# Performance work log

Measured on AMD Instinct MI355X. Metric: run time of the kernel, lower is better.

The kernel has to match this reference:

```python
import jax, jax.numpy as jnp
import numpy as np

H, KD, VD = 8, 64, 64
W = 1.25  # custom weight scale


def layer_norm(x, g, b, eps=1e-5):
    m = x.mean(-1, keepdims=True)
    v = ((x - m) ** 2).mean(-1, keepdims=True)
    return (x - m) * jax.lax.rsqrt(v + eps) * g + b


def cross_attention(x1, x2, wq, wk, wv, wo, bo, wm):
    # Conv1d kernel_size=1 == matmul; channel axis splits as (heads, dim)
    b, s1, _ = x1.shape
    s2 = x2.shape[1]
    q = (x1 @ wq.T).reshape(b, s1, H, KD).transpose(0, 2, 1, 3)  # bhqk
    k = (x2 @ wk.T).reshape(b, s2, H, KD).transpose(0, 2, 1, 3)
    v = (x2 @ wv.T).reshape(b, s2, H, VD).transpose(0, 2, 1, 3)
    attn = jnp.einsum('bhqd,bhsd->bhqs', q, k) * (1.0 / (KD ** 0.5))
    attn = jax.nn.softmax(attn * wm, axis=-1)  # elementwise weight BEFORE softmax
    o = jnp.einsum('bhqs,bhsv->bhqv', attn, v)
    o = o.transpose(0, 2, 1, 3).reshape(b, s1, H * VD)
    return o @ wo.T + bo


def make_wm1(nvars, sl2, patch_num):
    sl = sl2 // 2
    wm = jnp.ones((nvars, sl2), jnp.float32)
    wm = wm.at[:2 * patch_num, :sl].multiply(W)
    wm = wm.at[2 * patch_num:, sl:].multiply(W)
    return wm[None, None]  # broadcast over batch, heads


def make_wm2(nvars, sv, patch_num, patch_num_v):
    wm = jnp.ones((nvars, sv), jnp.float32)
    wm = wm.at[:patch_num, :patch_num_v].multiply(W)
    wm = wm.at[patch_num:2 * patch_num, patch_num_v:2 * patch_num_v].multiply(W)
    wm = wm.at[2 * patch_num:, 2 * patch_num_v:].multiply(W)
    return wm[None, None]


def forward(cords_features, spatial_features, speed_features,
            wq1, wk1, wv1, wo1, bo1, wq2, wk2, wv2, wo2, bo2,
            ln1_g, ln1_b, ln2_g, ln2_b, ln3_g, ln3_b,
            ffn_w1, ffn_b1, ffn_w2, ffn_b2):
    b, nvars, d = cords_features.shape
    patch_num = nvars // 3
    patch_num_v = speed_features.shape[1] // 3
    wm1 = make_wm1(nvars, spatial_features.shape[1], patch_num)
    wm2 = make_wm2(nvars, 3 * patch_num_v, patch_num, patch_num_v)
    x = cross_attention(cords_features, spatial_features, wq1, wk1, wv1, wo1, bo1, wm1)
    x = layer_norm(x + cords_features, ln1_g, ln1_b)
    r2 = x
    x = cross_attention(x, speed_features, wq2, wk2, wv2, wo2, bo2, wm2)
    x = layer_norm(x + r2, ln2_g, ln2_b)
    r3 = x
    h = jax.nn.gelu(x @ ffn_w1.T + ffn_b1, approximate=False)
    x = h @ ffn_w2.T + ffn_b2
    return layer_norm(x + r3, ln3_g, ln3_b)


def setup_inputs():
    key = jax.random.key(0)
    ks = jax.random.split(key, 16)
    D, DF = 512, 2048
    s = 0.02
    inp = {
        'cords_features': jax.random.normal(ks[0], (8, 768, D), jnp.float32),
        'spatial_features': jax.random.normal(ks[1], (8, 1024, D), jnp.float32),
        'speed_features': jax.random.normal(ks[2], (8, 768, D), jnp.float32),
        'wq1': jax.random.normal(ks[3], (H * KD, D)) * s,
        'wk1': jax.random.normal(ks[4], (H * KD, D)) * s,
        'wv1': jax.random.normal(ks[5], (H * VD, D)) * s,
        'wo1': jax.random.normal(ks[6], (D, H * VD)) * s,
        'bo1': jnp.zeros((D,), jnp.float32),
        'wq2': jax.random.normal(ks[7], (H * KD, D)) * s,
        'wk2': jax.random.normal(ks[8], (H * KD, D)) * s,
        'wv2': jax.random.normal(ks[9], (H * VD, D)) * s,
        'wo2': jax.random.normal(ks[10], (D, H * VD)) * s,
        'bo2': jnp.zeros((D,), jnp.float32),
        'ln1_g': jnp.ones((D,), jnp.float32), 'ln1_b': jnp.zeros((D,), jnp.float32),
        'ln2_g': jnp.ones((D,), jnp.float32), 'ln2_b': jnp.zeros((D,), jnp.float32),
        'ln3_g': jnp.ones((D,), jnp.float32), 'ln3_b': jnp.zeros((D,), jnp.float32),
        'ffn_w1': jax.random.normal(ks[11], (DF, D)) * s,
        'ffn_b1': jnp.zeros((DF,), jnp.float32),
        'ffn_w2': jax.random.normal(ks[12], (D, DF)) * s,
        'ffn_b2': jnp.zeros((D,), jnp.float32),
    }
    return inp


def reference(cords_features, spatial_features, speed_features,
              wq1, wk1, wv1, wo1, bo1, wq2, wk2, wv2, wo2, bo2,
              ln1_g, ln1_b, ln2_g, ln2_b, ln3_g, ln3_b,
              ffn_w1, ffn_b1, ffn_w2, ffn_b2):
    return forward(cords_features, spatial_features, speed_features,
                   wq1, wk1, wv1, wo1, bo1, wq2, wk2, wv2, wo2, bo2,
                   ln1_g, ln1_b, ln2_g, ln2_b, ln3_g, ln3_b,
                   ffn_w1, ffn_b1, ffn_w2, ffn_b2)
```

## Files before the change

### kernel.cpp

```cpp
#include <hip/hip_runtime.h>
#include <hip/hip_bf16.h>


#define LN_EPS 1e-5f
#define WSCALE 1.25f

typedef __attribute__((ext_vector_type(8))) short short8;
typedef __attribute__((ext_vector_type(4))) float floatx4;
typedef unsigned short us;

__device__ __forceinline__ float bf2f(us u) {
    union { unsigned int i; float f; } v; v.i = ((unsigned int)u) << 16; return v.f;
}
__device__ __forceinline__ us f2bf(float f) {
    union { float f; unsigned int i; } v; v.f = f;
    return (us)((v.i + 0x7FFFu + ((v.i >> 16) & 1u)) >> 16);
}
__device__ __forceinline__ float gelu_f(float v) {
    float x  = v * 0.70710678118654752f;
    float ax = fabsf(x);
    float t  = 1.0f / (1.0f + 0.3275911f * ax);
    float p  = t * (0.254829592f + t * (-0.284496736f + t * (1.421413741f +
               t * (-1.453152027f + t * 1.061405429f))));
    float er = 1.0f - p * __expf(-ax * ax);
    er = copysignf(er, x);
    return 0.5f * v * (1.0f + er);
}

__device__ __forceinline__ int xcd_swizzle_lid()
{
    int nwg = gridDim.x * gridDim.y;
    int lid = blockIdx.y * gridDim.x + blockIdx.x;
    int cpx = nwg >> 3;
    return (lid & 7) * cpx + (lid >> 3);
}

struct CastArgs {
    const float* src[13];
    us* dst[13];
    int blk_ofs[14];
};
__global__ __launch_bounds__(256) void cast_all(CastArgs a)
{
    int b = blockIdx.x;
    int e = 0;
    while (b >= a.blk_ofs[e + 1]) ++e;
    int i = ((b - a.blk_ofs[e]) * 256 + threadIdx.x) * 8;
    const float* s = a.src[e];
    us* d = a.dst[e];
    float4 x = *(const float4*)(s + i);
    float4 y = *(const float4*)(s + i + 4);
    *(ushort4*)(d + i)     = make_ushort4(f2bf(x.x), f2bf(x.y), f2bf(x.z), f2bf(x.w));
    *(ushort4*)(d + i + 4) = make_ushort4(f2bf(y.x), f2bf(y.y), f2bf(y.z), f2bf(y.w));
}

__global__ __launch_bounds__(256) void gemm_r64(
    const us* __restrict__ A, const us* __restrict__ Bw,
    const float* __restrict__ bias, us* __restrict__ Cb,
    int M, int N, int K, int flags)
{
    constexpr int BM = 128, BN = 64;
    constexpr int SLOT = (BM + BN) * 64;
    __shared__ us L[3 * SLOT];

    int t = threadIdx.x;
    int wave = t >> 6, lane = t & 63;

    int swz = xcd_swizzle_lid();
    int gx = gridDim.x;
    int m0 = (swz / gx) * BM, n0 = (swz % gx) * BN;

    int wr = wave * 32;

    int r_in = lane >> 3, pq = lane & 7;
    const us* gA[4]; int lA[4];
#pragma unroll
    for (int c = 0; c < 4; ++c) {
        int r = 32 * c + 8 * wave + r_in;
        int q = pq ^ (r & 7);
        gA[c] = A + (size_t)(m0 + r) * K + 8 * q;
        lA[c] = (32 * c + 8 * wave) * 64;
    }
    const us* gB[2]; int lB[2];
#pragma unroll
    for (int c = 0; c < 2; ++c) {
        int r = 32 * c + 8 * wave + r_in;
        int q = pq ^ (r & 7);
        gB[c] = Bw + (size_t)(n0 + r) * K + 8 * q;
        lB[c] = BM * 64 + (32 * c + 8 * wave) * 64;
    }

    int fcol = lane & 15, fj = lane >> 4;
    int aoff[2][2], boff[4][2];
#pragma unroll
    for (int mt = 0; mt < 2; ++mt)
#pragma unroll
        for (int kc = 0; kc < 2; ++kc) {
            int fr = wr + 16 * mt + fcol;
            aoff[mt][kc] = fr * 64 + ((kc * 4 + fj) ^ (fr & 7)) * 8;
        }
#pragma unroll
    for (int nt = 0; nt < 4; ++nt)
#pragma unroll
        for (int kc = 0; kc < 2; ++kc) {
            int br = 16 * nt + fcol;
            boff[nt][kc] = BM * 64 + br * 64 + ((kc * 4 + fj) ^ (br & 7)) * 8;
        }

    floatx4 acc[2][4] = {};

    auto stage_p0 = [&](int slot, int kt) {
        us* base = L + slot * SLOT;
#pragma unroll
        for (int c = 0; c < 3; ++c)
            __builtin_amdgcn_global_load_lds(
                (const __attribute__((address_space(1))) void*)(gA[c] + (size_t)kt * 64),
                (__attribute__((address_space(3))) void*)(base + lA[c]), 16, 0, 0);
    };
    auto stage_p1 = [&](int slot, int kt) {
        us* base = L + slot * SLOT;
        __builtin_amdgcn_global_load_lds(
            (const __attribute__((address_space(1))) void*)(gA[3] + (size_t)kt * 64),
            (__attribute__((address_space(3))) void*)(base + lA[3]), 16, 0, 0);
#pragma unroll
        for (int c = 0; c < 2; ++c)
            __builtin_amdgcn_global_load_lds(
                (const __attribute__((address_space(1))) void*)(gB[c] + (size_t)kt * 64),
                (__attribute__((address_space(3))) void*)(base + lB[c]), 16, 0, 0);
    };

    int ktrips = K >> 6;
    stage_p0(0, 0); stage_p1(0, 0);
    if (ktrips > 1) {
        stage_p0(1, 1); stage_p1(1, 1);
        asm volatile("s_waitcnt vmcnt(6)" ::: "memory");
    } else {
        asm volatile("s_waitcnt vmcnt(0)" ::: "memory");
    }
    __builtin_amdgcn_s_barrier();
    asm volatile("" ::: "memory");

    int cs = 0;
    for (int tt = 0; tt < ktrips; ++tt) {
        int ns = cs + 2; if (ns >= 3) ns -= 3;
        bool pre = (tt + 2) < ktrips;
        const us* base = L + cs * SLOT;

        if (pre) stage_p0(ns, tt + 2);
        {
            short8 af[2], bfv[4];
#pragma unroll
            for (int mt = 0; mt < 2; ++mt) af[mt] = *(const short8*)(base + aoff[mt][0]);
#pragma unroll
            for (int nt = 0; nt < 4; ++nt) bfv[nt] = *(const short8*)(base + boff[nt][0]);
            __builtin_amdgcn_s_setprio(1);
#pragma unroll
            for (int mt = 0; mt < 2; ++mt)
#pragma unroll
                for (int nt = 0; nt < 4; ++nt)
                    acc[mt][nt] = __builtin_amdgcn_mfma_f32_16x16x32_bf16(
                        af[mt], bfv[nt], acc[mt][nt], 0, 0, 0);
            __builtin_amdgcn_s_setprio(0);
        }

        if (pre) stage_p1(ns, tt + 2);
        {
            short8 af[2], bfv[4];
#pragma unroll
            for (int mt = 0; mt < 2; ++mt) af[mt] = *(const short8*)(base + aoff[mt][1]);
#pragma unroll
            for (int nt = 0; nt < 4; ++nt) bfv[nt] = *(const short8*)(base + boff[nt][1]);
            __builtin_amdgcn_s_setprio(1);
#pragma unroll
            for (int mt = 0; mt < 2; ++mt)
#pragma unroll
                for (int nt = 0; nt < 4; ++nt)
                    acc[mt][nt] = __builtin_amdgcn_mfma_f32_16x16x32_bf16(
                        af[mt], bfv[nt], acc[mt][nt], 0, 0, 0);
            __builtin_amdgcn_s_setprio(0);
        }

        if (tt + 1 < ktrips) {
            if (pre) asm volatile("s_waitcnt vmcnt(6)" ::: "memory");
            else     asm volatile("s_waitcnt vmcnt(0)" ::: "memory");
            __builtin_amdgcn_s_barrier();
            asm volatile("" ::: "memory");
        }
        cs = cs + 1; if (cs >= 3) cs = 0;
    }

    int rq = lane >> 4;
#pragma unroll
    for (int mt = 0; mt < 2; ++mt)
#pragma unroll
        for (int nt = 0; nt < 4; ++nt) {
            int col = n0 + 16 * nt + fcol;
            float bv = (flags & 1) ? bias[col] : 0.f;
#pragma unroll
            for (int r = 0; r < 4; ++r) {
                int row = m0 + wr + 16 * mt + rq * 4 + r;
                float v = acc[mt][nt][r] + bv;
                if (flags & 2) v = gelu_f(v);
                Cb[(size_t)row * N + col] = f2bf(v);
            }
        }
}

template<int BM, int BN>
__global__ __launch_bounds__(512, 2) void gemm_ring(
    const us* __restrict__ A, const us* __restrict__ Bw,
    const float* __restrict__ bias, us* __restrict__ Cb,
    int M, int N, int K, int flags, int vS, us* __restrict__ Vtg)
{
    static_assert(BM == 256 && BN == 128, "gemm_ring fixed at 256x128");
    constexpr int SLOT = (BM + BN) * 64;
    __shared__ us L[3 * SLOT];

    int t = threadIdx.x;
    int wave = t >> 6, lane = t & 63;

    int swz = xcd_swizzle_lid();
    int gx = gridDim.x;
    int m0 = (swz / gx) * BM, n0 = (swz % gx) * BN;

    int wr = (wave >> 1) * 64, wc = (wave & 1) * 64;

    int r_in = lane >> 3, pq = lane & 7;
    const us* gA[4]; int lA[4];
#pragma unroll
    for (int c = 0; c < 4; ++c) {
        int r = 64 * c + 8 * wave + r_in;
        int q = pq ^ (r & 7);
        gA[c] = A + (size_t)(m0 + r) * K + 8 * q;
        lA[c] = (64 * c + 8 * wave) * 64;
    }
    const us* gB[2]; int lB[2];
#pragma unroll
    for (int c = 0; c < 2; ++c) {
        int r = 64 * c + 8 * wave + r_in;
        int q = pq ^ (r & 7);
        gB[c] = Bw + (size_t)(n0 + r) * K + 8 * q;
        lB[c] = BM * 64 + (64 * c + 8 * wave) * 64;
    }

    int fcol = lane & 15, fj = lane >> 4;
    int aoff[4][2], boff[4][2];
#pragma unroll
    for (int mt = 0; mt < 4; ++mt)
#pragma unroll
        for (int kc = 0; kc < 2; ++kc) {
            int fr = wr + 16 * mt + fcol;
            aoff[mt][kc] = fr * 64 + ((kc * 4 + fj) ^ (fr & 7)) * 8;
        }
#pragma unroll
    for (int nt = 0; nt < 4; ++nt)
#pragma unroll
        for (int kc = 0; kc < 2; ++kc) {
            int br = wc + 16 * nt + fcol;
            boff[nt][kc] = BM * 64 + br * 64 + ((kc * 4 + fj) ^ (br & 7)) * 8;
        }

    floatx4 acc[4][4] = {};

    auto stage_p0 = [&](int slot, int kt) {
        us* base = L + slot * SLOT;
#pragma unroll
        for (int c = 0; c < 3; ++c)
            __builtin_amdgcn_global_load_lds(
                (const __attribute__((address_space(1))) void*)(gA[c] + (size_t)kt * 64),
                (__attribute__((address_space(3))) void*)(base + lA[c]), 16, 0, 0);
    };
    auto stage_p1 = [&](int slot, int kt) {
        us* base = L + slot * SLOT;
        __builtin_amdgcn_global_load_lds(
            (const __attribute__((address_space(1))) void*)(gA[3] + (size_t)kt * 64),
            (__attribute__((address_space(3))) void*)(base + lA[3]), 16, 0, 0);
#pragma unroll
        for (int c = 0; c < 2; ++c)
            __builtin_amdgcn_global_load_lds(
                (const __attribute__((address_space(1))) void*)(gB[c] + (size_t)kt * 64),
                (__attribute__((address_space(3))) void*)(base + lB[c]), 16, 0, 0);
    };

    int ktrips = K >> 6;
    stage_p0(0, 0); stage_p1(0, 0);
    if (ktrips > 1) {
        stage_p0(1, 1); stage_p1(1, 1);
        asm volatile("s_waitcnt vmcnt(6)" ::: "memory");
    } else {
        asm volatile("s_waitcnt vmcnt(0)" ::: "memory");
    }
    __builtin_amdgcn_s_barrier();
    asm volatile("" ::: "memory");

    int cs = 0;
    for (int tt = 0; tt < ktrips; ++tt) {
        int ns = cs + 2; if (ns >= 3) ns -= 3;
        bool pre = (tt + 2) < ktrips;
        const us* base = L + cs * SLOT;

        if (pre) stage_p0(ns, tt + 2);
        {
            short8 af[4], bfv[4];
#pragma unroll
            for (int mt = 0; mt < 4; ++mt) af[mt] = *(const short8*)(base + aoff[mt][0]);
#pragma unroll
            for (int nt = 0; nt < 4; ++nt) bfv[nt] = *(const short8*)(base + boff[nt][0]);
            __builtin_amdgcn_s_setprio(1);
#pragma unroll
            for (int mt = 0; mt < 4; ++mt)
#pragma unroll
                for (int nt = 0; nt < 4; ++nt)
                    acc[mt][nt] = __builtin_amdgcn_mfma_f32_16x16x32_bf16(
                        af[mt], bfv[nt], acc[mt][nt], 0, 0, 0);
            __builtin_amdgcn_s_setprio(0);
        }

        if (pre) stage_p1(ns, tt + 2);
        {
            short8 af[4], bfv[4];
#pragma unroll
            for (int mt = 0; mt < 4; ++mt) af[mt] = *(const short8*)(base + aoff[mt][1]);
#pragma unroll
            for (int nt = 0; nt < 4; ++nt) bfv[nt] = *(const short8*)(base + boff[nt][1]);
            __builtin_amdgcn_s_setprio(1);
#pragma unroll
            for (int mt = 0; mt < 4; ++mt)
#pragma unroll
                for (int nt = 0; nt < 4; ++nt)
                    acc[mt][nt] = __builtin_amdgcn_mfma_f32_16x16x32_bf16(
                        af[mt], bfv[nt], acc[mt][nt], 0, 0, 0);
            __builtin_amdgcn_s_setprio(0);
        }

        if (tt + 1 < ktrips) {
            if (pre) asm volatile("s_waitcnt vmcnt(6)" ::: "memory");
            else     asm volatile("s_waitcnt vmcnt(0)" ::: "memory");
            __builtin_amdgcn_s_barrier();
            asm volatile("" ::: "memory");
        }
        cs = cs + 1; if (cs >= 3) cs = 0;
    }

    int rq = lane >> 4;
    if (flags & 8) {
        int b = m0 / vS;
        int s_base = m0 - b * vS;
        if (n0 < 512) {
#pragma unroll
            for (int mt = 0; mt < 4; ++mt)
#pragma unroll
                for (int nt = 0; nt < 4; ++nt) {
                    int col = n0 + wc + 16 * nt + fcol;
#pragma unroll
                    for (int r = 0; r < 4; ++r) {
                        int rloc = wr + 16 * mt + rq * 4 + r;
                        Cb[(size_t)(m0 + rloc) * 512 + col] = f2bf(acc[mt][nt][r]);
                    }
                }
        } else {
#pragma unroll
            for (int mt = 0; mt < 4; ++mt)
#pragma unroll
                for (int nt = 0; nt < 4; ++nt) {
                    int cv = n0 + wc + 16 * nt + fcol - 512;
                    int hv = cv >> 6, dv = cv & 63;
                    int sb = s_base + wr + 16 * mt + rq * 4;
                    ushort4 pk = make_ushort4(
                        f2bf(acc[mt][nt][0]), f2bf(acc[mt][nt][1]),
                        f2bf(acc[mt][nt][2]), f2bf(acc[mt][nt][3]));
                    *(ushort4*)(Vtg + ((size_t)(b * 8 + hv) * 64 + dv) * vS + sb) = pk;
                }
        }
        return;
    }

#pragma unroll
    for (int mt = 0; mt < 4; ++mt)
#pragma unroll
        for (int nt = 0; nt < 4; ++nt) {
            int col = n0 + wc + 16 * nt + fcol;
            float bv = (flags & 1) ? bias[col] : 0.f;
#pragma unroll
            for (int r = 0; r < 4; ++r) {
                int row = m0 + wr + 16 * mt + rq * 4 + r;
                float v = acc[mt][nt][r] + bv;
                if (flags & 2) v = gelu_f(v);
                Cb[(size_t)row * N + col] = f2bf(v);
            }
        }
}

__global__ __launch_bounds__(256, 3) void attn_kernel(
    const us* __restrict__ Q, const us* __restrict__ Kf,
    const us* __restrict__ Vg, us* __restrict__ O,
    int S1, int S2, int shift)
{
    __shared__ us Qs[64 * 64];
    __shared__ us Ks[2][64 * 64];
    __shared__ us Vs[2][64 * 64];
    __shared__ us Ps[64 * 72];

    int t = threadIdx.x;
    int wave = t >> 6, lane = t & 63;
    int quad = lane >> 4, l15 = lane & 15;
    int q0 = blockIdx.x * 64, hh = blockIdx.y, bb = blockIdx.z;
    int qb = wave * 16;

    int r_in = lane >> 3, pq = lane & 7;
    const us *gK[2], *gV[2];
    int lofs[2];
#pragma unroll
    for (int c2 = 0; c2 < 2; ++c2) {
        int r = qb + 8 * c2 + r_in;
        int lq = pq ^ (r & 7);
        const us* gQ = Q + ((size_t)bb * S1 + q0 + r) * 512 + hh * 64 + 8 * lq;
        gK[c2] = Kf + ((size_t)bb * S2 + r) * 512 + hh * 64 + 8 * lq;
        gV[c2] = Vg + ((size_t)(bb * 8 + hh) * 64 + r) * S2 + 8 * lq;
        lofs[c2] = (qb + 8 * c2) * 64;
        __builtin_amdgcn_global_load_lds(
            (const __attribute__((address_space(1))) void*)gQ,
            (__attribute__((address_space(3))) void*)(Qs + lofs[c2]), 16, 0, 0);
    }

    int aoffQ[2], poffP[2], boff[4][2];
#pragma unroll
    for (int kc = 0; kc < 2; ++kc) {
        int ph = ((kc * 4 + quad) ^ (l15 & 7)) * 8;
        aoffQ[kc] = (qb + l15) * 64 + ph;
        poffP[kc] = (qb + l15) * 72 + ph;
#pragma unroll
        for (int nt = 0; nt < 4; ++nt)
            boff[nt][kc] = (16 * nt + l15) * 64 + ph;
    }
    int pwoff[4][4];
#pragma unroll
    for (int r = 0; r < 4; ++r) {
        int row = qb + quad * 4 + r;
#pragma unroll
        for (int nt = 0; nt < 4; ++nt) {
            int s = 16 * nt + l15;
            pwoff[nt][r] = row * 72 + (((s >> 3) ^ (row & 7)) * 8) + (s & 7);
        }
    }

    floatx4 acc_o[4] = {};
    float l_part[4] = {0.f, 0.f, 0.f, 0.f};
    int qsh[4];
#pragma unroll
    for (int r = 0; r < 4; ++r) qsh[r] = (q0 + qb + quad * 4 + r) >> shift;

    auto stageKV = [&](int buf, int cc) {
#pragma unroll
        for (int c2 = 0; c2 < 2; ++c2) {
            __builtin_amdgcn_global_load_lds(
                (const __attribute__((address_space(1))) void*)(gK[c2] + (size_t)cc * 512),
                (__attribute__((address_space(3))) void*)(Ks[buf] + lofs[c2]), 16, 0, 0);
            __builtin_amdgcn_global_load_lds(
                (const __attribute__((address_space(1))) void*)(gV[c2] + cc),
                (__attribute__((address_space(3))) void*)(Vs[buf] + lofs[c2]), 16, 0, 0);
        }
    };

    stageKV(0, 0);
    asm volatile("s_waitcnt vmcnt(4)" ::: "memory");
    __builtin_amdgcn_s_barrier();
    asm volatile("" ::: "memory");
    short8 aq0 = *(const short8*)(Qs + aoffQ[0]);
    short8 aq1 = *(const short8*)(Qs + aoffQ[1]);

    int ntile = S2 >> 6;
    for (int ti = 0; ti < ntile; ++ti) {
        int buf = ti & 1;
        if (ti + 1 < ntile) {
            stageKV(buf ^ 1, (ti + 1) << 6);
            asm volatile("s_waitcnt vmcnt(4)" ::: "memory");
        } else {
            asm volatile("s_waitcnt vmcnt(0)" ::: "memory");
        }
        __builtin_amdgcn_s_barrier();
        asm volatile("" ::: "memory");

        const us* ks_ = Ks[buf];
        const us* vs_ = Vs[buf];
        int cbase = ti << 6;

        floatx4 s_acc[4] = {};
#pragma unroll
        for (int nt = 0; nt < 4; ++nt) {
            short8 bk0 = *(const short8*)(ks_ + boff[nt][0]);
            short8 bk1 = *(const short8*)(ks_ + boff[nt][1]);
            s_acc[nt] = __builtin_amdgcn_mfma_f32_16x16x32_bf16(aq0, bk0, s_acc[nt], 0, 0, 0);
            s_acc[nt] = __builtin_amdgcn_mfma_f32_16x16x32_bf16(aq1, bk1, s_acc[nt], 0, 0, 0);
        }

#pragma unroll
        for (int nt = 0; nt < 4; ++nt) {
            int srs = (cbase + 16 * nt + l15) >> shift;
#pragma unroll
            for (int r = 0; r < 4; ++r) {
                float fct = (qsh[r] == srs) ? (0.125f * WSCALE) : 0.125f;
                float p = __expf(s_acc[nt][r] * fct);
                s_acc[nt][r] = p;
                l_part[r] += p;
            }
        }

#pragma unroll
        for (int nt = 0; nt < 4; ++nt)
#pragma unroll
            for (int r = 0; r < 4; ++r)
                Ps[pwoff[nt][r]] = f2bf(s_acc[nt][r]);
        __builtin_amdgcn_wave_barrier();

        short8 ap0 = *(const short8*)(Ps + poffP[0]);
        short8 ap1 = *(const short8*)(Ps + poffP[1]);
#pragma unroll
        for (int nt = 0; nt < 4; ++nt) {
            short8 bv0 = *(const short8*)(vs_ + boff[nt][0]);
            short8 bv1 = *(const short8*)(vs_ + boff[nt][1]);
            acc_o[nt] = __builtin_amdgcn_mfma_f32_16x16x32_bf16(ap0, bv0, acc_o[nt], 0, 0, 0);
            acc_o[nt] = __builtin_amdgcn_mfma_f32_16x16x32_bf16(ap1, bv1, acc_o[nt], 0, 0, 0);
        }

        asm volatile("" ::: "memory");
        __builtin_amdgcn_s_barrier();
    }

#pragma unroll
    for (int r = 0; r < 4; ++r) {
#pragma unroll
        for (int off = 8; off; off >>= 1)
            l_part[r] += __shfl_xor(l_part[r], off, 16);
    }
#pragma unroll
    for (int r = 0; r < 4; ++r) {
        float inv = 1.0f / l_part[r];
        size_t base = ((size_t)bb * S1 + q0 + qb + quad * 4 + r) * 512 + hh * 64;
#pragma unroll
        for (int nt = 0; nt < 4; ++nt)
            O[base + 16 * nt + l15] = f2bf(acc_o[nt][r] * inv);
    }
}

__global__ __launch_bounds__(256) void ln_kernel(
    const us* __restrict__ X, const float* __restrict__ R,
    const float* __restrict__ g, const float* __restrict__ bta,
    float* __restrict__ out, us* __restrict__ outb)
{
    int row = blockIdx.x;
    int t   = threadIdx.x;
    const us*    xr = X + (size_t)row * 512;
    const float* rr = R + (size_t)row * 512;
    float v0 = bf2f(xr[t]) + rr[t];
    float v1 = bf2f(xr[t + 256]) + rr[t + 256];
    float s  = v0 + v1;
    float sq = v0 * v0 + v1 * v1;
#pragma unroll
    for (int off = 32; off; off >>= 1) {
        s  += __shfl_xor(s, off, 64);
        sq += __shfl_xor(sq, off, 64);
    }
    __shared__ float ps[4], psq[4];
    int w = t >> 6;
    if ((t & 63) == 0) { ps[w] = s; psq[w] = sq; }
    __syncthreads();
    float S  = ps[0] + ps[1] + ps[2] + ps[3];
    float SQ = psq[0] + psq[1] + psq[2] + psq[3];
    float mean = S * (1.0f / 512.0f);
    float var  = SQ * (1.0f / 512.0f) - mean * mean;
    float inv  = rsqrtf(var + LN_EPS);
    float y0 = (v0 - mean) * inv * g[t] + bta[t];
    float y1 = (v1 - mean) * inv * g[t + 256] + bta[t + 256];
    out[(size_t)row * 512 + t]       = y0;
    out[(size_t)row * 512 + t + 256] = y1;
    if (outb) {
        outb[(size_t)row * 512 + t]       = f2bf(y0);
        outb[(size_t)row * 512 + t + 256] = f2bf(y1);
    }
}

extern "C" void kernel_launch(void* const* d_in, const int* in_sizes, int n_in,
                              void* d_out, int out_size, void* d_ws, size_t ws_size,
                              hipStream_t stream)
{
    const float* cords   = (const float*)d_in[0];
    const float* spatial = (const float*)d_in[1];
    const float* speed   = (const float*)d_in[2];
    const float* wq1 = (const float*)d_in[3];
    const float* wk1 = (const float*)d_in[4];
    const float* wv1 = (const float*)d_in[5];
    const float* wo1 = (const float*)d_in[6];
    const float* bo1 = (const float*)d_in[7];
    const float* wq2 = (const float*)d_in[8];
    const float* wk2 = (const float*)d_in[9];
    const float* wv2 = (const float*)d_in[10];
    const float* wo2 = (const float*)d_in[11];
    const float* bo2 = (const float*)d_in[12];
    const float* ln1g = (const float*)d_in[13];
    const float* ln1b = (const float*)d_in[14];
    const float* ln2g = (const float*)d_in[15];
    const float* ln2b = (const float*)d_in[16];
    const float* ln3g = (const float*)d_in[17];
    const float* ln3b = (const float*)d_in[18];
    const float* fw1 = (const float*)d_in[19];
    const float* fb1 = (const float*)d_in[20];
    const float* fw2 = (const float*)d_in[21];
    const float* fb2 = (const float*)d_in[22];

    const int B = 8, S1 = 768, S2 = 1024, Sv = 768, D = 512, DF = 2048;
    const int M1 = B * S1;
    const int M2 = B * S2;

    char* w = (char*)d_ws;
    us* q_bf = (us*)w;              w += (size_t)M1 * D * 2;
    us* k_bf = (us*)w;              w += (size_t)M2 * D * 2;
    us* vt   = (us*)w;              w += (size_t)M2 * D * 2;
    us* o_bf = (us*)w;              w += (size_t)M1 * D * 2;
    us* p_bf = (us*)w;              w += (size_t)M1 * D * 2;
    float* x1 = (float*)w;          w += (size_t)M1 * D * 4;
    us* cords_bf   = (us*)w;        w += (size_t)M1 * D * 2;
    us* spatial_bf = (us*)w;        w += (size_t)M2 * D * 2;
    us* speed_bf   = (us*)w;        w += (size_t)M1 * D * 2;
    us* wq1b = (us*)w;              w += (size_t)D * D * 2;
    us* wk1b = (us*)w;              w += (size_t)D * D * 2;
    us* wv1b = (us*)w;              w += (size_t)D * D * 2;
    us* wo1b = (us*)w;              w += (size_t)D * D * 2;
    us* wq2b = (us*)w;              w += (size_t)D * D * 2;
    us* wk2b = (us*)w;              w += (size_t)D * D * 2;
    us* wv2b = (us*)w;              w += (size_t)D * D * 2;
    us* wo2b = (us*)w;              w += (size_t)D * D * 2;
    us* fw1b = (us*)w;              w += (size_t)DF * D * 2;
    us* fw2b = (us*)w;              w += (size_t)DF * D * 2;

    us* h_bf  = q_bf;
    us* y_bf  = p_bf;
    us* x1_bf = spatial_bf;
    us* x2_bf = cords_bf;
    float* x2 = (float*)d_out;

    dim3 blk(256);
    dim3 blk512(512);

    {
        CastArgs ca;
        const float* srcs[13] = {cords, spatial, speed, wq1, wk1, wv1, wo1,
                                 wq2, wk2, wv2, wo2, fw1, fw2};
        us* dsts[13] = {cords_bf, spatial_bf, speed_bf, wq1b, wk1b, wv1b, wo1b,
                        wq2b, wk2b, wv2b, wo2b, fw1b, fw2b};
        int ns[13] = {M1 * D, M2 * D, M1 * D, D * D, D * D, D * D, D * D,
                      D * D, D * D, D * D, D * D, DF * D, DF * D};
        int ofs = 0;
        for (int i = 0; i < 13; ++i) {
            ca.src[i] = srcs[i]; ca.dst[i] = dsts[i];
            ca.blk_ofs[i] = ofs; ofs += ns[i] / 2048;
        }
        ca.blk_ofs[13] = ofs;
        cast_all<<<dim3(ofs), blk, 0, stream>>>(ca);
    }

    auto gr64  = [](int M, int N) { return dim3(N / 64,  M / 128); };
    auto gring = [](int M, int N) { return dim3(N / 128, M / 256); };

    gemm_r64<<<gr64(M1, D), blk, 0, stream>>>(cords_bf, wq1b, nullptr, q_bf, M1, D, D, 0);
    gemm_ring<256, 128><<<gring(M2, 1024), blk512, 0, stream>>>(spatial_bf, wk1b, nullptr, k_bf,
                                                                M2, 1024, D, 8, S2, vt);
    attn_kernel<<<dim3(S1 / 64, 8, B), blk, 0, stream>>>(q_bf, k_bf, vt, o_bf, S1, S2, 9);
    gemm_r64<<<gr64(M1, D), blk, 0, stream>>>(o_bf, wo1b, bo1, p_bf, M1, D, D, 1);
    ln_kernel<<<M1, blk, 0, stream>>>(p_bf, cords, ln1g, ln1b, x1, x1_bf);

    gemm_r64<<<gr64(M1, D), blk, 0, stream>>>(x1_bf, wq2b, nullptr, q_bf, M1, D, D, 0);
    gemm_ring<256, 128><<<gring(M1, 1024), blk512, 0, stream>>>(speed_bf, wk2b, nullptr, k_bf,
                                                                M1, 1024, D, 8, Sv, vt);
    attn_kernel<<<dim3(S1 / 64, 8, B), blk, 0, stream>>>(q_bf, k_bf, vt, o_bf, S1, Sv, 8);
    gemm_r64<<<gr64(M1, D), blk, 0, stream>>>(o_bf, wo2b, bo2, p_bf, M1, D, D, 1);
    ln_kernel<<<M1, blk, 0, stream>>>(p_bf, x1, ln2g, ln2b, x2, x2_bf);

    gemm_ring<256, 128><<<gring(M1, DF), blk512, 0, stream>>>(x2_bf, fw1b, fb1, h_bf,
                                                              M1, DF, D, 1 | 2 | 4, 0, nullptr);
    gemm_r64<<<gr64(M1, D), blk, 0, stream>>>(h_bf, fw2b, fb2, y_bf, M1, D, DF, 1);
    ln_kernel<<<M1, blk, 0, stream>>>(y_bf, x2, ln3g, ln3b, (float*)d_out, nullptr);

    (void)in_sizes; (void)n_in; (void)out_size; (void)ws_size;
}
```

Before: 333.7 us.

## Process 128 query rows per attention block to reuse K/V tiles

The attention kernel now handles 128 query rows per block, with each wave computing two 16-row M-tiles, instead of 64 rows. Each K/V tile staged in LDS, and each K/V fragment read from it, now feeds twice as many MFMAs. This halves K/V global traffic and staging per query. In exchange, the grid has half as many blocks, and the LDS and register footprints grow, so the launch-bounds occupancy hint drops from 3 to 2.

```diff
diff --git a/kernel.cpp b/kernel.cpp
--- a/kernel.cpp
+++ b/kernel.cpp
@@ -391,64 +391,84 @@
         }
 }
 
-__global__ __launch_bounds__(256, 3) void attn_kernel(
+__global__ __launch_bounds__(256, 2) void attn_kernel(
     const us* __restrict__ Q, const us* __restrict__ Kf,
     const us* __restrict__ Vg, us* __restrict__ O,
     int S1, int S2, int shift)
 {
-    __shared__ us Qs[64 * 64];
+    __shared__ us Qs[128 * 64];
     __shared__ us Ks[2][64 * 64];
     __shared__ us Vs[2][64 * 64];
-    __shared__ us Ps[64 * 72];
+    __shared__ us Ps[128 * 72];
 
     int t = threadIdx.x;
     int wave = t >> 6, lane = t & 63;
     int quad = lane >> 4, l15 = lane & 15;
-    int q0 = blockIdx.x * 64, hh = blockIdx.y, bb = blockIdx.z;
+    int q0 = blockIdx.x * 128, hh = blockIdx.y, bb = blockIdx.z;
     int qb = wave * 16;
+    int wq = wave * 32;
 
     int r_in = lane >> 3, pq = lane & 7;
+
+#pragma unroll
+    for (int c = 0; c < 4; ++c) {
+        int r = 32 * c + 8 * wave + r_in;
+        int lq = pq ^ (r & 7);
+        const us* gQ = Q + ((size_t)bb * S1 + q0 + r) * 512 + hh * 64 + 8 * lq;
+        __builtin_amdgcn_global_load_lds(
+            (const __attribute__((address_space(1))) void*)gQ,
+            (__attribute__((address_space(3))) void*)(Qs + (32 * c + 8 * wave) * 64), 16, 0, 0);
+    }
+
     const us *gK[2], *gV[2];
     int lofs[2];
 #pragma unroll
     for (int c2 = 0; c2 < 2; ++c2) {
         int r = qb + 8 * c2 + r_in;
         int lq = pq ^ (r & 7);
-        const us* gQ = Q + ((size_t)bb * S1 + q0 + r) * 512 + hh * 64 + 8 * lq;
         gK[c2] = Kf + ((size_t)bb * S2 + r) * 512 + hh * 64 + 8 * lq;
         gV[c2] = Vg + ((size_t)(bb * 8 + hh) * 64 + r) * S2 + 8 * lq;
         lofs[c2] = (qb + 8 * c2) * 64;
-        __builtin_amdgcn_global_load_lds(
-            (const __attribute__((address_space(1))) void*)gQ,
-            (__attribute__((address_space(3))) void*)(Qs + lofs[c2]), 16, 0, 0);
-    }
-
-    int aoffQ[2], poffP[2], boff[4][2];
-#pragma unroll
-    for (int kc = 0; kc < 2; ++kc) {
-        int ph = ((kc * 4 + quad) ^ (l15 & 7)) * 8;
-        aoffQ[kc] = (qb + l15) * 64 + ph;
-        poffP[kc] = (qb + l15) * 72 + ph;
-#pragma unroll
-        for (int nt = 0; nt < 4; ++nt)
-            boff[nt][kc] = (16 * nt + l15) * 64 + ph;
-    }
-    int pwoff[4][4];
-#pragma unroll
-    for (int r = 0; r < 4; ++r) {
-        int row = qb + quad * 4 + r;
-#pragma unroll
-        for (int nt = 0; nt < 4; ++nt) {
-            int s = 16 * nt + l15;
-            pwoff[nt][r] = row * 72 + (((s >> 3) ^ (row & 7)) * 8) + (s & 7);
-        }
-    }
-
-    floatx4 acc_o[4] = {};
-    float l_part[4] = {0.f, 0.f, 0.f, 0.f};
-    int qsh[4];
-#pragma unroll
-    for (int r = 0; r < 4; ++r) qsh[r] = (q0 + qb + quad * 4 + r) >> shift;
+    }
+
+    int aoffQ[2][2], poffP[2][2], boff[4][2];
+#pragma unroll
+    for (int mt = 0; mt < 2; ++mt)
+#pragma unroll
+        for (int kc = 0; kc < 2; ++kc) {
+            int fr = wq + 16 * mt + l15;
+            int ph = ((kc * 4 + quad) ^ (fr & 7)) * 8;
+            aoffQ[mt][kc] = fr * 64 + ph;
+            poffP[mt][kc] = fr * 72 + ph;
+        }
+#pragma unroll
+    for (int nt = 0; nt < 4; ++nt)
+#pragma unroll
+        for (int kc = 0; kc < 2; ++kc) {
+            int br = 16 * nt + l15;
+            boff[nt][kc] = br * 64 + ((kc * 4 + quad) ^ (br & 7)) * 8;
+        }
+    int pwoff[2][4][4];
+#pragma unroll
+    for (int mt = 0; mt < 2; ++mt)
+#pragma unroll
+        for (int r = 0; r < 4; ++r) {
+            int row = wq + 16 * mt + quad * 4 + r;
+#pragma unroll
+            for (int nt = 0; nt < 4; ++nt) {
+                int s = 16 * nt + l15;
+                pwoff[mt][nt][r] = row * 72 + (((s >> 3) ^ (row & 7)) * 8) + (s & 7);
+            }
+        }
+
+    floatx4 acc_o[2][4] = {};
+    float l_part[2][4] = {};
+    int qsh[2][4];
+#pragma unroll
+    for (int mt = 0; mt < 2; ++mt)
+#pragma unroll
+        for (int r = 0; r < 4; ++r)
+            qsh[mt][r] = (q0 + wq + 16 * mt + quad * 4 + r) >> shift;
 
     auto stageKV = [&](int buf, int cc) {
 #pragma unroll
@@ -466,8 +486,12 @@
     asm volatile("s_waitcnt vmcnt(4)" ::: "memory");
     __builtin_amdgcn_s_barrier();
     asm volatile("" ::: "memory");
-    short8 aq0 = *(const short8*)(Qs + aoffQ[0]);
-    short8 aq1 = *(const short8*)(Qs + aoffQ[1]);
+    short8 aq[2][2];
+#pragma unroll
+    for (int mt = 0; mt < 2; ++mt)
+#pragma unroll
+        for (int kc = 0; kc < 2; ++kc)
+            aq[mt][kc] = *(const short8*)(Qs + aoffQ[mt][kc]);
 
     int ntile = S2 >> 6;
     for (int ti = 0; ti < ntile; ++ti) {
@@ -485,42 +509,60 @@
         const us* vs_ = Vs[buf];
         int cbase = ti << 6;
 
-        floatx4 s_acc[4] = {};
+        floatx4 s_acc[2][4] = {};
 #pragma unroll
         for (int nt = 0; nt < 4; ++nt) {
             short8 bk0 = *(const short8*)(ks_ + boff[nt][0]);
             short8 bk1 = *(const short8*)(ks_ + boff[nt][1]);
-            s_acc[nt] = __builtin_amdgcn_mfma_f32_16x16x32_bf16(aq0, bk0, s_acc[nt], 0, 0, 0);
-            s_acc[nt] = __builtin_amdgcn_mfma_f32_16x16x32_bf16(aq1, bk1, s_acc[nt], 0, 0, 0);
+#pragma unroll
+            for (int mt = 0; mt < 2; ++mt) {
+                s_acc[mt][nt] = __builtin_amdgcn_mfma_f32_16x16x32_bf16(
+                    aq[mt][0], bk0, s_acc[mt][nt], 0, 0, 0);
+                s_acc[mt][nt] = __builtin_amdgcn_mfma_f32_16x16x32_bf16(
+                    aq[mt][1], bk1, s_acc[mt][nt], 0, 0, 0);
+            }
         }
 
 #pragma unroll
         for (int nt = 0; nt < 4; ++nt) {
             int srs = (cbase + 16 * nt + l15) >> shift;
 #pragma unroll
-            for (int r = 0; r < 4; ++r) {
-                float fct = (qsh[r] == srs) ? (0.125f * WSCALE) : 0.125f;
-                float p = __expf(s_acc[nt][r] * fct);
-                s_acc[nt][r] = p;
-                l_part[r] += p;
-            }
-        }
-
-#pragma unroll
-        for (int nt = 0; nt < 4; ++nt)
-#pragma unroll
-            for (int r = 0; r < 4; ++r)
-                Ps[pwoff[nt][r]] = f2bf(s_acc[nt][r]);
+            for (int mt = 0; mt < 2; ++mt)
+#pragma unroll
+                for (int r = 0; r < 4; ++r) {
+                    float fct = (qsh[mt][r] == srs) ? (0.125f * WSCALE) : 0.125f;
+                    float p = __expf(s_acc[mt][nt][r] * fct);
+                    s_acc[mt][nt][r] = p;
+                    l_part[mt][r] += p;
+                }
+        }
+
+#pragma unroll
+        for (int mt = 0; mt < 2; ++mt)
+#pragma unroll
+            for (int nt = 0; nt < 4; ++nt)
+#pragma unroll
+                for (int r = 0; r < 4; ++r)
+                    Ps[pwoff[mt][nt][r]] = f2bf(s_acc[mt][nt][r]);
         __builtin_amdgcn_wave_barrier();
 
-        short8 ap0 = *(const short8*)(Ps + poffP[0]);
-        short8 ap1 = *(const short8*)(Ps + poffP[1]);
+        short8 ap[2][2];
+#pragma unroll
+        for (int mt = 0; mt < 2; ++mt) {
+            ap[mt][0] = *(const short8*)(Ps + poffP[mt][0]);
+            ap[mt][1] = *(const short8*)(Ps + poffP[mt][1]);
+        }
 #pragma unroll
         for (int nt = 0; nt < 4; ++nt) {
             short8 bv0 = *(const short8*)(vs_ + boff[nt][0]);
             short8 bv1 = *(const short8*)(vs_ + boff[nt][1]);
-            acc_o[nt] = __builtin_amdgcn_mfma_f32_16x16x32_bf16(ap0, bv0, acc_o[nt], 0, 0, 0);
-            acc_o[nt] = __builtin_amdgcn_mfma_f32_16x16x32_bf16(ap1, bv1, acc_o[nt], 0, 0, 0);
+#pragma unroll
+            for (int mt = 0; mt < 2; ++mt) {
+                acc_o[mt][nt] = __builtin_amdgcn_mfma_f32_16x16x32_bf16(
+                    ap[mt][0], bv0, acc_o[mt][nt], 0, 0, 0);
+                acc_o[mt][nt] = __builtin_amdgcn_mfma_f32_16x16x32_bf16(
+                    ap[mt][1], bv1, acc_o[mt][nt], 0, 0, 0);
+            }
         }
 
         asm volatile("" ::: "memory");
@@ -528,19 +570,23 @@
     }
 
 #pragma unroll
-    for (int r = 0; r < 4; ++r) {
-#pragma unroll
-        for (int off = 8; off; off >>= 1)
-            l_part[r] += __shfl_xor(l_part[r], off, 16);
-    }
-#pragma unroll
-    for (int r = 0; r < 4; ++r) {
-        float inv = 1.0f / l_part[r];
-        size_t base = ((size_t)bb * S1 + q0 + qb + quad * 4 + r) * 512 + hh * 64;
-#pragma unroll
-        for (int nt = 0; nt < 4; ++nt)
-            O[base + 16 * nt + l15] = f2bf(acc_o[nt][r] * inv);
-    }
+    for (int mt = 0; mt < 2; ++mt)
+#pragma unroll
+        for (int r = 0; r < 4; ++r) {
+#pragma unroll
+            for (int off = 8; off; off >>= 1)
+                l_part[mt][r] += __shfl_xor(l_part[mt][r], off, 16);
+        }
+#pragma unroll
+    for (int mt = 0; mt < 2; ++mt)
+#pragma unroll
+        for (int r = 0; r < 4; ++r) {
+            float inv = 1.0f / l_part[mt][r];
+            size_t base = ((size_t)bb * S1 + q0 + wq + 16 * mt + quad * 4 + r) * 512 + hh * 64;
+#pragma unroll
+            for (int nt = 0; nt < 4; ++nt)
+                O[base + 16 * nt + l15] = f2bf(acc_o[mt][nt][r] * inv);
+        }
 }
 
 __global__ __launch_bounds__(256) void ln_kernel(
@@ -665,14 +711,14 @@
     gemm_r64<<<gr64(M1, D), blk, 0, stream>>>(cords_bf, wq1b, nullptr, q_bf, M1, D, D, 0);
     gemm_ring<256, 128><<<gring(M2, 1024), blk512, 0, stream>>>(spatial_bf, wk1b, nullptr, k_bf,
                                                                 M2, 1024, D, 8, S2, vt);
-    attn_kernel<<<dim3(S1 / 64, 8, B), blk, 0, stream>>>(q_bf, k_bf, vt, o_bf, S1, S2, 9);
+    attn_kernel<<<dim3(S1 / 128, 8, B), blk, 0, stream>>>(q_bf, k_bf, vt, o_bf, S1, S2, 9);
     gemm_r64<<<gr64(M1, D), blk, 0, stream>>>(o_bf, wo1b, bo1, p_bf, M1, D, D, 1);
     ln_kernel<<<M1, blk, 0, stream>>>(p_bf, cords, ln1g, ln1b, x1, x1_bf);
 
     gemm_r64<<<gr64(M1, D), blk, 0, stream>>>(x1_bf, wq2b, nullptr, q_bf, M1, D, D, 0);
     gemm_ring<256, 128><<<gring(M1, 1024), blk512, 0, stream>>>(speed_bf, wk2b, nullptr, k_bf,
                                                                 M1, 1024, D, 8, Sv, vt);
-    attn_kernel<<<dim3(S1 / 64, 8, B), blk, 0, stream>>>(q_bf, k_bf, vt, o_bf, S1, Sv, 8);
+    attn_kernel<<<dim3(S1 / 128, 8, B), blk, 0, stream>>>(q_bf, k_bf, vt, o_bf, S1, Sv, 8);
     gemm_r64<<<gr64(M1, D), blk, 0, stream>>>(o_bf, wo2b, bo2, p_bf, M1, D, D, 1);
     ln_kernel<<<M1, blk, 0, stream>>>(p_bf, x1, ln2g, ln2b, x2, x2_bf);
 
```

New measurement: 343.5 us. 1.03x slower.
